# Kernel optimization log

Hardware: AMD Instinct MI355X
Metric: run time of the kernel (lower is better)

Reference implementation:

```python
import jax, jax.numpy as jnp
import numpy as np
from jax import lax

B, T, C = 64, 1024, 512
INIT_P = 1.0
CLAMP_LO, CLAMP_HI = 1e-4, 1.0 - 1e-4


def setup_inputs() -> dict:
    key = jax.random.key(0)
    k1, k2 = jax.random.split(key)
    x = jax.random.normal(k1, (B, T, C), dtype=jnp.float32)
    # learnable per-channel logit(lambda); original inits to logit(0.98) repeated,
    # use randn around that value so gradients are nontrivial
    init_logit = float(np.log(0.98 / (1.0 - 0.98)))
    logit_lambda = init_logit + 0.1 * jax.random.normal(k2, (C,), dtype=jnp.float32)
    return {"x": x, "logit_lambda": logit_lambda}


def reference(x, logit_lambda):
    # lam: [C] -> broadcast over (B, C) states
    lam = jnp.clip(jax.nn.sigmoid(logit_lambda), CLAMP_LO, CLAMP_HI)
    theta0 = x[:, 0, :]                                   # [B, C]
    P0 = jnp.full(theta0.shape, INIT_P, dtype=x.dtype)    # [B, C]

    def step(carry, xt):
        theta, P = carry
        K = P / (lam + P)                 # gain, data-independent of x
        theta = theta + K * (xt - theta)  # level update
        P = (P - K * P) / lam             # covariance update
        return (theta, P), theta

    xs = jnp.swapaxes(x, 0, 1)[1:]        # [T-1, B, C], timesteps 1..T-1
    _, ys = lax.scan(step, (theta0, P0), xs)
    # y[:,0,:] = x[:,0,:], y[:,t,:] = theta_t for t>=1
    y = jnp.concatenate([theta0[:, None, :], jnp.swapaxes(ys, 0, 1)], axis=1)
    return y
```

## Files before the change

### kernel.cpp

```cpp
#include <hip/hip_runtime.h>
#include <math.h>


namespace {
constexpr int kB = 64;
constexpr int kT = 1024;
constexpr int kC = 512;
constexpr int kNCH = 16;
constexpr int kL = kT / kNCH;
constexpr int kCV = kC / 4;
constexpr int kChunks = kB * kNCH;
constexpr int kBlocks = kChunks / 2;
constexpr size_t kCarryOffB = 1024;
constexpr size_t kCarryU64 = (size_t)kChunks * kCV * 4;
}

typedef float vfloat4 __attribute__((ext_vector_type(4)));

__device__ __forceinline__ void load_lam(const float* __restrict__ zl, int c0,
                                         float lam[4]) {
  vfloat4 z = *reinterpret_cast<const vfloat4*>(zl + c0);
#pragma unroll
  for (int k = 0; k < 4; ++k) {
    float s = 1.0f / (1.0f + expf(-z[k]));
    lam[k] = fminf(fmaxf(s, 1e-4f), 1.0f - 1e-4f);
  }
}

__device__ __forceinline__ float poll_val(
    const unsigned long long* __restrict__ p) {
  unsigned long long u = __hip_atomic_load(p, __ATOMIC_RELAXED,
                                           __HIP_MEMORY_SCOPE_AGENT);
  while (!(u >> 32)) {
    __builtin_amdgcn_s_sleep(1);
    u = __hip_atomic_load(p, __ATOMIC_RELAXED, __HIP_MEMORY_SCOPE_AGENT);
  }
  union { unsigned u32; float f; } c;
  c.u32 = (unsigned)u;
  return c.f;
}

extern "C" __global__ __launch_bounds__(256) void ewrls_init(
    unsigned long long* __restrict__ cw, unsigned* __restrict__ tk) {
  size_t i = (size_t)blockIdx.x * 256 + threadIdx.x;
  if (i < kCarryU64) cw[i] = 0ull;
  if (i == 0) *tk = 0u;
}

extern "C" __global__ __launch_bounds__(256) void ewrls_fused(
    const float* __restrict__ x, const float* __restrict__ zl,
    unsigned* __restrict__ ws, float* __restrict__ y) {
  __shared__ unsigned sh_t;
  if (threadIdx.x == 0)
    sh_t = __hip_atomic_fetch_add(ws, 1u, __ATOMIC_RELAXED,
                                  __HIP_MEMORY_SCOPE_AGENT);
  __syncthreads();
  const unsigned T = sh_t;
  const int c = (int)(2u * T) + (int)(threadIdx.x >> 7);
  const int j = c >> 6;
  const int b = c & 63;
  const int cv = threadIdx.x & 127;

  unsigned long long* __restrict__ carry =
      reinterpret_cast<unsigned long long*>(
          reinterpret_cast<char*>(ws) + kCarryOffB);

  float lam[4];
  load_lam(zl, cv * 4, lam);

  const size_t base = ((size_t)b * kT + (size_t)j * kL) * kCV + cv;
  const vfloat4* xp = reinterpret_cast<const vfloat4*>(x) + base;
  float a0 = 0.f, a1 = 0.f, a2 = 0.f, a3 = 0.f;
#pragma unroll 8
  for (int t = 0; t < kL; ++t) {
    vfloat4 v = xp[(size_t)t * kCV];
    a0 = fmaf(lam[0], a0, v.x);
    a1 = fmaf(lam[1], a1, v.y);
    a2 = fmaf(lam[2], a2, v.z);
    a3 = fmaf(lam[3], a3, v.w);
  }

  {
    unsigned long long* cp = carry + (((size_t)c * kCV + cv) << 2);
    union { float f; unsigned u; } q;
    q.f = a0;
    __hip_atomic_store(cp + 0, (1ull << 32) | q.u, __ATOMIC_RELAXED,
                       __HIP_MEMORY_SCOPE_AGENT);
    q.f = a1;
    __hip_atomic_store(cp + 1, (1ull << 32) | q.u, __ATOMIC_RELAXED,
                       __HIP_MEMORY_SCOPE_AGENT);
    q.f = a2;
    __hip_atomic_store(cp + 2, (1ull << 32) | q.u, __ATOMIC_RELAXED,
                       __HIP_MEMORY_SCOPE_AGENT);
    q.f = a3;
    __hip_atomic_store(cp + 3, (1ull << 32) | q.u, __ATOMIC_RELAXED,
                       __HIP_MEMORY_SCOPE_AGENT);
  }

  float lamL[4];
#pragma unroll
  for (int k = 0; k < 4; ++k) {
    float p = lam[k];
#pragma unroll
    for (int q = 0; q < 6; ++q) p = p * p;
    lamL[k] = p;
  }

  float S0 = 0.f, S1 = 0.f, S2 = 0.f, S3 = 0.f;
  float p0 = 1.f, p1 = 1.f, p2 = 1.f, p3 = 1.f;
  for (int i = 0; i < j; ++i) {
    const unsigned long long* cp =
        carry + ((((size_t)i * kB + b) * kCV + cv) << 2);
    float v0 = poll_val(cp + 0);
    float v1 = poll_val(cp + 1);
    float v2 = poll_val(cp + 2);
    float v3 = poll_val(cp + 3);
    S0 = fmaf(lamL[0], S0, v0);
    S1 = fmaf(lamL[1], S1, v1);
    S2 = fmaf(lamL[2], S2, v2);
    S3 = fmaf(lamL[3], S3, v3);
    p0 *= lamL[0];
    p1 *= lamL[1];
    p2 *= lamL[2];
    p3 *= lamL[3];
  }

  float Q0 = (1.0f - p0) * __builtin_amdgcn_rcpf(1.0f - lam[0]);
  float Q1 = (1.0f - p1) * __builtin_amdgcn_rcpf(1.0f - lam[1]);
  float Q2 = (1.0f - p2) * __builtin_amdgcn_rcpf(1.0f - lam[2]);
  float Q3 = (1.0f - p3) * __builtin_amdgcn_rcpf(1.0f - lam[3]);

  vfloat4* yp = reinterpret_cast<vfloat4*>(y) + base;
#pragma unroll 8
  for (int t = 0; t < kL; ++t) {
    vfloat4 v = __builtin_nontemporal_load(&xp[(size_t)t * kCV]);
    S0 = fmaf(lam[0], S0, v.x);
    S1 = fmaf(lam[1], S1, v.y);
    S2 = fmaf(lam[2], S2, v.z);
    S3 = fmaf(lam[3], S3, v.w);
    Q0 = fmaf(lam[0], Q0, 1.0f);
    Q1 = fmaf(lam[1], Q1, 1.0f);
    Q2 = fmaf(lam[2], Q2, 1.0f);
    Q3 = fmaf(lam[3], Q3, 1.0f);
    vfloat4 o;
    o.x = S0 * __builtin_amdgcn_rcpf(Q0);
    o.y = S1 * __builtin_amdgcn_rcpf(Q1);
    o.z = S2 * __builtin_amdgcn_rcpf(Q2);
    o.w = S3 * __builtin_amdgcn_rcpf(Q3);
    __builtin_nontemporal_store(o, &yp[(size_t)t * kCV]);
  }
}

extern "C" __global__ __launch_bounds__(256) void ewrls_serial(
    const float* __restrict__ x, const float* __restrict__ zl,
    float* __restrict__ y) {
  int idx = blockIdx.x * 256 + threadIdx.x;
  int cv = idx % kCV;
  int b = idx / kCV;
  float lam[4];
  load_lam(zl, cv * 4, lam);
  float S[4] = {0.f, 0.f, 0.f, 0.f};
  float Q[4] = {0.f, 0.f, 0.f, 0.f};
  const size_t base = (size_t)b * kT * kCV + cv;
  const vfloat4* xp = reinterpret_cast<const vfloat4*>(x) + base;
  vfloat4* yp = reinterpret_cast<vfloat4*>(y) + base;
#pragma unroll 4
  for (int t = 0; t < kT; ++t) {
    vfloat4 v = xp[(size_t)t * kCV];
    S[0] = fmaf(lam[0], S[0], v.x);
    S[1] = fmaf(lam[1], S[1], v.y);
    S[2] = fmaf(lam[2], S[2], v.z);
    S[3] = fmaf(lam[3], S[3], v.w);
    Q[0] = fmaf(lam[0], Q[0], 1.0f);
    Q[1] = fmaf(lam[1], Q[1], 1.0f);
    Q[2] = fmaf(lam[2], Q[2], 1.0f);
    Q[3] = fmaf(lam[3], Q[3], 1.0f);
    vfloat4 o;
    o.x = S[0] * __builtin_amdgcn_rcpf(Q[0]);
    o.y = S[1] * __builtin_amdgcn_rcpf(Q[1]);
    o.z = S[2] * __builtin_amdgcn_rcpf(Q[2]);
    o.w = S[3] * __builtin_amdgcn_rcpf(Q[3]);
    yp[(size_t)t * kCV] = o;
  }
}

extern "C" void kernel_launch(void* const* d_in, const int* in_sizes, int n_in,
                              void* d_out, int out_size, void* d_ws,
                              size_t ws_size, hipStream_t stream) {
  const float* x = (const float*)d_in[0];
  const float* zl = (const float*)d_in[1];
  float* y = (float*)d_out;

  const size_t need = kCarryOffB + kCarryU64 * 8;
  if (ws_size >= need) {
    unsigned* ws = (unsigned*)d_ws;
    unsigned long long* cw = reinterpret_cast<unsigned long long*>(
        reinterpret_cast<char*>(d_ws) + kCarryOffB);
    ewrls_init<<<(int)((kCarryU64 + 255) / 256), 256, 0, stream>>>(cw, ws);
    ewrls_fused<<<kBlocks, 256, 0, stream>>>(x, zl, ws, y);
  } else {
    const int n = kB * kCV;
    ewrls_serial<<<n / 256, 256, 0, stream>>>(x, zl, y);
  }
}
```

Baseline: 257.5 us.

## Stage chunk rows in LDS, shrink chunks, and batch carry polling

Chunks shrink from 64 to 32 timesteps, giving one chunk per block and 2048 blocks. Each block stages its 32x512 input tile in LDS, so x is read from global memory once instead of twice. The two half-blocks split the output pass, with the second half rebuilding its starting state from the first-half partial sum. Carry polling now issues loads for four predecessor chunks before waiting on them, which cuts serialized latency. The costs are a longer cross-chunk lookback chain (up to 31 predecessors), 64KB of LDS per block that limits occupancy, and plain stores replacing nontemporal ones.

```diff
diff --git a/kernel.cpp b/kernel.cpp
--- a/kernel.cpp
+++ b/kernel.cpp
@@ -6,11 +6,10 @@
 constexpr int kB = 64;
 constexpr int kT = 1024;
 constexpr int kC = 512;
-constexpr int kNCH = 16;
-constexpr int kL = kT / kNCH;
+constexpr int kRows = 32;
+constexpr int kNJ = kT / kRows;
 constexpr int kCV = kC / 4;
-constexpr int kChunks = kB * kNCH;
-constexpr int kBlocks = kChunks / 2;
+constexpr int kChunks = kB * kNJ;
 constexpr size_t kCarryOffB = 1024;
 constexpr size_t kCarryU64 = (size_t)kChunks * kCV * 4;
 }
@@ -27,17 +26,9 @@
   }
 }
 
-__device__ __forceinline__ float poll_val(
+__device__ __forceinline__ unsigned long long ld_carry(
     const unsigned long long* __restrict__ p) {
-  unsigned long long u = __hip_atomic_load(p, __ATOMIC_RELAXED,
-                                           __HIP_MEMORY_SCOPE_AGENT);
-  while (!(u >> 32)) {
-    __builtin_amdgcn_s_sleep(1);
-    u = __hip_atomic_load(p, __ATOMIC_RELAXED, __HIP_MEMORY_SCOPE_AGENT);
-  }
-  union { unsigned u32; float f; } c;
-  c.u32 = (unsigned)u;
-  return c.f;
+  return __hip_atomic_load(p, __ATOMIC_RELAXED, __HIP_MEMORY_SCOPE_AGENT);
 }
 
 extern "C" __global__ __launch_bounds__(256) void ewrls_init(
@@ -51,15 +42,16 @@
     const float* __restrict__ x, const float* __restrict__ zl,
     unsigned* __restrict__ ws, float* __restrict__ y) {
   __shared__ unsigned sh_t;
+  __shared__ vfloat4 lds_x[kRows * kCV];
   if (threadIdx.x == 0)
     sh_t = __hip_atomic_fetch_add(ws, 1u, __ATOMIC_RELAXED,
                                   __HIP_MEMORY_SCOPE_AGENT);
   __syncthreads();
-  const unsigned T = sh_t;
-  const int c = (int)(2u * T) + (int)(threadIdx.x >> 7);
+  const int c = (int)sh_t;
   const int j = c >> 6;
   const int b = c & 63;
-  const int cv = threadIdx.x & 127;
+  const int cv = (int)(threadIdx.x & 127);
+  const int h = (int)(threadIdx.x >> 7);
 
   unsigned long long* __restrict__ carry =
       reinterpret_cast<unsigned long long*>(
@@ -68,72 +60,124 @@
   float lam[4];
   load_lam(zl, cv * 4, lam);
 
-  const size_t base = ((size_t)b * kT + (size_t)j * kL) * kCV + cv;
-  const vfloat4* xp = reinterpret_cast<const vfloat4*>(x) + base;
-  float a0 = 0.f, a1 = 0.f, a2 = 0.f, a3 = 0.f;
+  const size_t cbase = ((size_t)b * kT + (size_t)j * kRows) * kCV;
+  const vfloat4* xp = reinterpret_cast<const vfloat4*>(x) + cbase;
 #pragma unroll 8
-  for (int t = 0; t < kL; ++t) {
-    vfloat4 v = xp[(size_t)t * kCV];
-    a0 = fmaf(lam[0], a0, v.x);
-    a1 = fmaf(lam[1], a1, v.y);
-    a2 = fmaf(lam[2], a2, v.z);
-    a3 = fmaf(lam[3], a3, v.w);
-  }
-
-  {
+  for (int it = 0; it < 16; ++it) {
+    const int o = it * 256 + (int)threadIdx.x;
+    lds_x[o] = xp[o];
+  }
+  __syncthreads();
+
+  float A0 = 0.f, A1 = 0.f, A2 = 0.f, A3 = 0.f;
+#pragma unroll 8
+  for (int t = 0; t < 16; ++t) {
+    vfloat4 v = lds_x[t * kCV + cv];
+    A0 = fmaf(lam[0], A0, v.x);
+    A1 = fmaf(lam[1], A1, v.y);
+    A2 = fmaf(lam[2], A2, v.z);
+    A3 = fmaf(lam[3], A3, v.w);
+  }
+  const float L0 = A0, L1 = A1, L2 = A2, L3 = A3;
+#pragma unroll 8
+  for (int t = 16; t < kRows; ++t) {
+    vfloat4 v = lds_x[t * kCV + cv];
+    A0 = fmaf(lam[0], A0, v.x);
+    A1 = fmaf(lam[1], A1, v.y);
+    A2 = fmaf(lam[2], A2, v.z);
+    A3 = fmaf(lam[3], A3, v.w);
+  }
+
+  if (h == 0) {
     unsigned long long* cp = carry + (((size_t)c * kCV + cv) << 2);
     union { float f; unsigned u; } q;
-    q.f = a0;
+    q.f = A0;
     __hip_atomic_store(cp + 0, (1ull << 32) | q.u, __ATOMIC_RELAXED,
                        __HIP_MEMORY_SCOPE_AGENT);
-    q.f = a1;
+    q.f = A1;
     __hip_atomic_store(cp + 1, (1ull << 32) | q.u, __ATOMIC_RELAXED,
                        __HIP_MEMORY_SCOPE_AGENT);
-    q.f = a2;
+    q.f = A2;
     __hip_atomic_store(cp + 2, (1ull << 32) | q.u, __ATOMIC_RELAXED,
                        __HIP_MEMORY_SCOPE_AGENT);
-    q.f = a3;
+    q.f = A3;
     __hip_atomic_store(cp + 3, (1ull << 32) | q.u, __ATOMIC_RELAXED,
                        __HIP_MEMORY_SCOPE_AGENT);
   }
 
-  float lamL[4];
+  float l16[4], l32[4];
 #pragma unroll
   for (int k = 0; k < 4; ++k) {
     float p = lam[k];
-#pragma unroll
-    for (int q = 0; q < 6; ++q) p = p * p;
-    lamL[k] = p;
-  }
-
-  float S0 = 0.f, S1 = 0.f, S2 = 0.f, S3 = 0.f;
+    p = p * p; p = p * p; p = p * p; p = p * p;
+    l16[k] = p;
+    l32[k] = p * p;
+  }
+
+  float G0 = 0.f, G1 = 0.f, G2 = 0.f, G3 = 0.f;
   float p0 = 1.f, p1 = 1.f, p2 = 1.f, p3 = 1.f;
-  for (int i = 0; i < j; ++i) {
-    const unsigned long long* cp =
-        carry + ((((size_t)i * kB + b) * kCV + cv) << 2);
-    float v0 = poll_val(cp + 0);
-    float v1 = poll_val(cp + 1);
-    float v2 = poll_val(cp + 2);
-    float v3 = poll_val(cp + 3);
-    S0 = fmaf(lamL[0], S0, v0);
-    S1 = fmaf(lamL[1], S1, v1);
-    S2 = fmaf(lamL[2], S2, v2);
-    S3 = fmaf(lamL[3], S3, v3);
-    p0 *= lamL[0];
-    p1 *= lamL[1];
-    p2 *= lamL[2];
-    p3 *= lamL[3];
-  }
-
-  float Q0 = (1.0f - p0) * __builtin_amdgcn_rcpf(1.0f - lam[0]);
-  float Q1 = (1.0f - p1) * __builtin_amdgcn_rcpf(1.0f - lam[1]);
-  float Q2 = (1.0f - p2) * __builtin_amdgcn_rcpf(1.0f - lam[2]);
-  float Q3 = (1.0f - p3) * __builtin_amdgcn_rcpf(1.0f - lam[3]);
-
-  vfloat4* yp = reinterpret_cast<vfloat4*>(y) + base;
-#pragma unroll 8
-  for (int t = 0; t < kL; ++t) {
-    vfloat4 v = __builtin_nontemporal_load(&xp[(size_t)t * kCV]);
+  for (int i0 = 0; i0 < j; i0 += 4) {
+    const int n = j - i0;
+    unsigned long long u[4][4];
+#pragma unroll
+    for (int k = 0; k < 4; ++k) {
+      if (k < n) {
+        const unsigned long long* cp =
+            carry + ((((size_t)(i0 + k) * kB + b) * kCV + cv) << 2);
+        u[k][0] = ld_carry(cp + 0);
+        u[k][1] = ld_carry(cp + 1);
+        u[k][2] = ld_carry(cp + 2);
+        u[k][3] = ld_carry(cp + 3);
+      }
+    }
+#pragma unroll
+    for (int k = 0; k < 4; ++k) {
+      if (k < n) {
+        const unsigned long long* cp =
+            carry + ((((size_t)(i0 + k) * kB + b) * kCV + cv) << 2);
+        while (!((u[k][0] >> 32) & (u[k][1] >> 32) & (u[k][2] >> 32) &
+                 (u[k][3] >> 32))) {
+          __builtin_amdgcn_s_sleep(2);
+          u[k][0] = ld_carry(cp + 0);
+          u[k][1] = ld_carry(cp + 1);
+          u[k][2] = ld_carry(cp + 2);
+          u[k][3] = ld_carry(cp + 3);
+        }
+        union { unsigned uu; float f; } w;
+        w.uu = (unsigned)u[k][0]; G0 = fmaf(l32[0], G0, w.f);
+        w.uu = (unsigned)u[k][1]; G1 = fmaf(l32[1], G1, w.f);
+        w.uu = (unsigned)u[k][2]; G2 = fmaf(l32[2], G2, w.f);
+        w.uu = (unsigned)u[k][3]; G3 = fmaf(l32[3], G3, w.f);
+        p0 *= l32[0];
+        p1 *= l32[1];
+        p2 *= l32[2];
+        p3 *= l32[3];
+      }
+    }
+  }
+
+  float S0, S1, S2, S3, pq0, pq1, pq2, pq3;
+  if (h == 0) {
+    S0 = G0; S1 = G1; S2 = G2; S3 = G3;
+    pq0 = p0; pq1 = p1; pq2 = p2; pq3 = p3;
+  } else {
+    S0 = fmaf(l16[0], G0, L0);
+    S1 = fmaf(l16[1], G1, L1);
+    S2 = fmaf(l16[2], G2, L2);
+    S3 = fmaf(l16[3], G3, L3);
+    pq0 = p0 * l16[0]; pq1 = p1 * l16[1];
+    pq2 = p2 * l16[2]; pq3 = p3 * l16[3];
+  }
+  float Q0 = (1.0f - pq0) * __builtin_amdgcn_rcpf(1.0f - lam[0]);
+  float Q1 = (1.0f - pq1) * __builtin_amdgcn_rcpf(1.0f - lam[1]);
+  float Q2 = (1.0f - pq2) * __builtin_amdgcn_rcpf(1.0f - lam[2]);
+  float Q3 = (1.0f - pq3) * __builtin_amdgcn_rcpf(1.0f - lam[3]);
+
+  const int r0 = h * 16;
+  vfloat4* yp = reinterpret_cast<vfloat4*>(y) + cbase;
+#pragma unroll 4
+  for (int t = 0; t < 16; ++t) {
+    vfloat4 v = lds_x[(r0 + t) * kCV + cv];
     S0 = fmaf(lam[0], S0, v.x);
     S1 = fmaf(lam[1], S1, v.y);
     S2 = fmaf(lam[2], S2, v.z);
@@ -147,7 +191,7 @@
     o.y = S1 * __builtin_amdgcn_rcpf(Q1);
     o.z = S2 * __builtin_amdgcn_rcpf(Q2);
     o.w = S3 * __builtin_amdgcn_rcpf(Q3);
-    __builtin_nontemporal_store(o, &yp[(size_t)t * kCV]);
+    yp[(size_t)(r0 + t) * kCV + cv] = o;
   }
 }
 
@@ -197,7 +241,7 @@
     unsigned long long* cw = reinterpret_cast<unsigned long long*>(
         reinterpret_cast<char*>(d_ws) + kCarryOffB);
     ewrls_init<<<(int)((kCarryU64 + 255) / 256), 256, 0, stream>>>(cw, ws);
-    ewrls_fused<<<kBlocks, 256, 0, stream>>>(x, zl, ws, y);
+    ewrls_fused<<<kChunks, 256, 0, stream>>>(x, zl, ws, y);
   } else {
     const int n = kB * kCV;
     ewrls_serial<<<n / 256, 256, 0, stream>>>(x, zl, y);
```

After: 276.0 us. 7.2% more time.
